# Kernel tuning notes

Hardware: AMD Instinct MI355X
Metric: run time of the kernel (lower is better)

## Reference

```python
import jax, jax.numpy as jnp
import numpy as np
from jax import lax

# MinkowskiEngine semantics reproduced on a dense grid:
# - a sparse tensor's active set = voxels where any feature channel is nonzero
# - stride-1 conv: output coords == input coords  -> mask output with input mask
# - stride-2 conv (k=5, pad=2): output coords = unique(floor(c/2))  -> 2x2x2 max-pool of mask
# - GlobalPooling: mean of features over active output coords, per batch
# MinkowskiConvolution has no bias by default; MinkowskiLinear has one.

DN = ('NCDHW', 'OIDHW', 'NCDHW')

def conv3d(x, w, stride, pad):
    return lax.conv_general_dilated(
        x, w, (stride, stride, stride), [(pad, pad)] * 3, dimension_numbers=DN)

def pool_mask(m):
    # occupancy of stride-2 output coords: any active voxel in each 2x2x2 block
    B, T, H, W = m.shape
    return m.reshape(B, T // 2, 2, H // 2, 2, W // 2, 2).max(axis=(2, 4, 6))

def setup_inputs() -> dict:
    key = jax.random.key(0)
    ks = jax.random.split(key, 7)
    B, T, C, H, W = 16, 128, 2, 34, 34
    vals = jax.random.normal(ks[0], (B, T, C, H, W), jnp.float32)
    keep = jax.random.bernoulli(ks[1], 0.05, (B, T, 1, H, W)).astype(jnp.float32)
    x = vals * keep
    w1 = jax.random.normal(ks[2], (32, 2, 5, 5, 5), jnp.float32) * 0.05
    w2 = jax.random.normal(ks[3], (64, 32, 5, 5, 5), jnp.float32) * 0.05
    w3 = jax.random.normal(ks[4], (128, 64, 3, 3, 3), jnp.float32) * 0.05
    wl = jax.random.normal(ks[5], (10, 128), jnp.float32) * 0.05
    bl = jnp.zeros((10,), jnp.float32)
    return {"x": x, "w1": w1, "w2": w2, "w3": w3, "wl": wl, "bl": bl}

def reference(x, w1, w2, w3, wl, bl):
    # x: [B, T, C, H, W] -> permute(0,2,1,3,4) -> [B, C, T, H, W]
    dense = jnp.transpose(x, (0, 2, 1, 3, 4))
    # active coordinate set of ME.to_sparse(dense)
    mask = (jnp.abs(dense).sum(axis=1) > 0).astype(dense.dtype)  # [B, T, H, W]
    mask = lax.stop_gradient(mask)
    m1 = mask[:, None]
    h = conv3d(dense, w1, 1, 2) * m1                         # k5 s1, out coords = in coords
    mask2 = pool_mask(mask)                                  # stride-2 output occupancy
    m2 = mask2[:, None]
    h = jax.nn.relu(conv3d(h, w2, 2, 2)) * m2                # k5 s2 + ReLU
    h = jax.nn.relu(conv3d(h, w3, 1, 1)) * m2                # k3 s1 + ReLU
    cnt = jnp.maximum(mask2.sum(axis=(1, 2, 3)), 1.0)[:, None]
    pooled = h.sum(axis=(2, 3, 4)) / cnt                     # global avg over active coords -> [B,128]
    logits = pooled @ wl.T + bl                              # MinkowskiLinear(128,10)
    return jax.nn.softmax(jax.nn.relu(logits), axis=-1)      # ReLU -> Softmax -> ToFeature [B,10]
```

## Files before the change

kernel.cpp:

```cpp
#include <hip/hip_runtime.h>

#define BB 16
#define TT 128
#define HH 34
#define WW 34
#define HWSZ (HH*WW)
#define NP1 (BB*TT*HH*WW)
#define TD 64
#define HD 17
#define WD 17
#define NP2 (BB*TD*HD*WD)
#define NW1 (NP1/64)
#define NW2 (NP2/64)
#define CAP1 262144
#define CAP2 131072

typedef __attribute__((ext_vector_type(8))) short bf16x8;
typedef __attribute__((ext_vector_type(4))) float f32x4;

__device__ inline unsigned short f2bf(float f) {
  unsigned u = __float_as_uint(f);
  unsigned r = (u + 0x7fff + ((u >> 16) & 1)) >> 16;
  return (unsigned short)r;
}
__device__ inline float bf2f(unsigned short s) {
  return __uint_as_float((unsigned)s << 16);
}

__global__ void k_ballot1(const float* __restrict__ x, unsigned long long* __restrict__ b1) {
  int i = blockIdx.x * 256 + threadIdx.x;
  int hw = i % HWSZ;
  int bt = i / HWSZ;
  const float* px = x + (size_t)bt * 2 * HWSZ + hw;
  bool act = (fabsf(px[0]) + fabsf(px[HWSZ])) > 0.0f;
  unsigned long long m = __ballot(act);
  if ((threadIdx.x & 63) == 0) b1[i >> 6] = m;
}

__global__ void k_ballot2(const unsigned long long* __restrict__ b1,
                          unsigned long long* __restrict__ b2) {
  int i = blockIdx.x * 256 + threadIdx.x;
  if (i >= NP2) return;
  int ow = i % WD; int r = i / WD;
  int oh = r % HD; r /= HD;
  int od = r % TD; int b = r / TD;
  bool act = false;
  for (int dt = 0; dt < 2; dt++)
    for (int dh = 0; dh < 2; dh++)
      for (int dw = 0; dw < 2; dw++) {
        int t = od * 2 + dt, h = oh * 2 + dh, w = ow * 2 + dw;
        int lin = ((b * TT + t) * HH + h) * WW + w;
        if ((b1[lin >> 6] >> (lin & 63)) & 1ull) act = true;
      }
  unsigned long long m = __ballot(act);
  if ((threadIdx.x & 63) == 0) b2[i >> 6] = m;
}

__global__ __launch_bounds__(1024) void k_scan(
    const unsigned long long* __restrict__ b1, const unsigned long long* __restrict__ b2,
    int* __restrict__ wb1, int* __restrict__ wb2,
    int* __restrict__ counter1, int* __restrict__ counter2, float* __restrict__ cnt) {
  __shared__ int wsum[16];
  __shared__ int wpre[16];
  __shared__ int tots[2];
  int tid = threadIdx.x, lane = tid & 63, wv = tid >> 6;

  const int CH1 = (NW1 + 1023) / 1024;
  int lo = tid * CH1, hi = min(lo + CH1, NW1);
  int s = 0;
  for (int i = lo; i < hi; i++) s += __popcll(b1[i]);
  int sc = s;
  #pragma unroll
  for (int d = 1; d < 64; d <<= 1) { int y = __shfl_up(sc, d); if (lane >= d) sc += y; }
  if (lane == 63) wsum[wv] = sc;
  __syncthreads();
  if (wv == 0 && lane < 16) {
    int v = wsum[lane];
    int p = v;
    #pragma unroll
    for (int d = 1; d < 16; d <<= 1) { int y = __shfl_up(p, d); if (lane >= d) p += y; }
    wpre[lane] = p - v;
    if (lane == 15) tots[0] = p;
  }
  __syncthreads();
  {
    int base = wpre[wv] + (sc - s);
    for (int i = lo; i < hi; i++) { wb1[i] = base; base += __popcll(b1[i]); }
  }
  if (tid == 0) *counter1 = tots[0];
  __syncthreads();

  const int CH2 = (NW2 + 1023) / 1024;
  lo = tid * CH2; hi = min(lo + CH2, NW2);
  s = 0;
  for (int i = lo; i < hi; i++) s += __popcll(b2[i]);
  sc = s;
  #pragma unroll
  for (int d = 1; d < 64; d <<= 1) { int y = __shfl_up(sc, d); if (lane >= d) sc += y; }
  if (lane == 63) wsum[wv] = sc;
  __syncthreads();
  if (wv == 0 && lane < 16) {
    int v = wsum[lane];
    int p = v;
    #pragma unroll
    for (int d = 1; d < 16; d <<= 1) { int y = __shfl_up(p, d); if (lane >= d) p += y; }
    wpre[lane] = p - v;
    if (lane == 15) tots[1] = p;
  }
  __syncthreads();
  {
    int base = wpre[wv] + (sc - s);
    for (int i = lo; i < hi; i++) { wb2[i] = base; base += __popcll(b2[i]); }
  }
  if (tid == 0) *counter2 = tots[1];
  __syncthreads();
  if (tid < 16) {
    int c0 = wb2[tid * 289];
    int c1 = (tid == 15) ? tots[1] : wb2[(tid + 1) * 289];
    cnt[tid] = (float)(c1 - c0);
  }
}

__global__ void k_fill1(const unsigned long long* __restrict__ b1,
                        const int* __restrict__ wb1, int* __restrict__ idx1) {
  int i = blockIdx.x * 256 + threadIdx.x;
  unsigned long long m = b1[i >> 6];
  int lane = i & 63;
  int p = -1;
  if ((m >> lane) & 1ull) {
    p = wb1[i >> 6] + __popcll(m & ((1ull << lane) - 1ull));
    if (p >= CAP1) p = -1;
  }
  idx1[i] = p;
}

__global__ void k_fill2(const unsigned long long* __restrict__ b2,
                        const int* __restrict__ wb2,
                        int* __restrict__ idx2, int* __restrict__ list2) {
  int i = blockIdx.x * 256 + threadIdx.x;
  if (i >= NP2) return;
  unsigned long long m = b2[i >> 6];
  int lane = i & 63;
  int p = -1;
  if ((m >> lane) & 1ull) {
    p = wb2[i >> 6] + __popcll(m & ((1ull << lane) - 1ull));
    if (p < CAP2) list2[p] = i; else p = -1;
  }
  idx2[i] = p;
}

__global__ __launch_bounds__(256) void k_conv1e(
    const float* __restrict__ x, const float* __restrict__ w1,
    const unsigned long long* __restrict__ b1, const int* __restrict__ wb1,
    unsigned short* __restrict__ h1c) {
  __shared__ unsigned short w1s[8000];
  __shared__ unsigned int plist[384];
  __shared__ unsigned long long q[4][128];
  __shared__ int pcnt;
  int tid = threadIdx.x;
  int b = blockIdx.x >> 7;
  int t0 = blockIdx.x & 127;
  if (tid == 0) pcnt = 0;
  for (int j = tid; j < 8000; j += 256) w1s[j] = f2bf(w1[j]);
  __syncthreads();
  int slabbase = (b * TT + t0) * HWSZ;
  for (int hw = tid; hw < HWSZ; hw += 256) {
    int lin = slabbase + hw;
    unsigned long long m = b1[lin >> 6];
    int ln = lin & 63;
    if ((m >> ln) & 1ull) {
      int p = wb1[lin >> 6] + __popcll(m & ((1ull << ln) - 1ull));
      if (p < CAP1) {
        int s = atomicAdd(&pcnt, 1);
        if (s < 384) plist[s] = ((unsigned)p << 11) | (unsigned)hw;
      }
    }
  }
  __syncthreads();
  int n = min(pcnt, 384);
  int lane = tid & 63, wid = tid >> 6;
  int oc = lane & 31, c = lane >> 5;
  int woff = (oc * 2 + c) * 125;
  int csh = c * 16;
  int kt = lane / 5, kh = lane - kt * 5;
  const float* xb = x + (size_t)b * TT * 2 * HWSZ;
  for (int li = wid; li < n; li += 4) {
    unsigned e = plist[li];
    int hw = e & 0x7ff;
    int p = e >> 11;
    int h_ = hw / 34, w_ = hw - h_ * 34;
    int cntA = 0;
    unsigned m5 = 0;
    int t2 = 0, h2 = 0;
    if (lane < 25) {
      t2 = t0 + kt - 2;
      h2 = h_ + kh - 2;
      if ((unsigned)t2 < TT && (unsigned)h2 < HH) {
        int kwmin = (w_ < 2) ? (2 - w_) : 0;
        int kwmax = (w_ > 31) ? (35 - w_) : 4;
        int lin = ((b * TT + t2) * HH + h2) * WW + (w_ + kwmin - 2);
        int wi = lin >> 6, sh = lin & 63;
        unsigned long long v = b1[wi] >> sh;
        if (sh > 59) v |= b1[wi + 1] << (64 - sh);
        m5 = ((unsigned)v & ((1u << (kwmax - kwmin + 1)) - 1u)) << kwmin;
        cntA = __popc(m5);
      }
    }
    int inc = cntA;
    #pragma unroll
    for (int d = 1; d < 64; d <<= 1) { int y = __shfl_up(inc, d); if (lane >= d) inc += y; }
    int off = inc - cntA;
    int ne = __shfl(inc, 63);
    unsigned mm = m5;
    while (mm) {
      int kw = __ffs(mm) - 1; mm &= mm - 1;
      int w2 = w_ + kw - 2;
      int xoff = (t2 * 2) * HWSZ + h2 * 34 + w2;
      unsigned short xv0 = f2bf(xb[xoff]);
      unsigned short xv1 = f2bf(xb[xoff + HWSZ]);
      int tap = (kt * 5 + kh) * 5 + kw;
      q[wid][off++] = (unsigned long long)((unsigned)xv0 | ((unsigned)xv1 << 16)) |
                      ((unsigned long long)tap << 32);
    }
    float acc = 0.f;
    for (int e2 = 0; e2 < ne; e2++) {
      unsigned long long ent = q[wid][e2];
      int tap = (int)(ent >> 32);
      float xv = bf2f((unsigned short)((ent >> csh) & 0xffffull));
      acc += xv * bf2f(w1s[woff + tap]);
    }
    float other = __shfl_down(acc, 32);
    if (lane < 32) h1c[(size_t)p * 32 + oc] = f2bf(acc + other);
  }
}

__global__ void k_tw2b(const float* __restrict__ w2, unsigned short* __restrict__ w2b) {
  int i = blockIdx.x * blockDim.x + threadIdx.x;
  if (i >= 125 * 64 * 32) return;
  int c = i & 31; int r = i >> 5;
  int oc = r & 63; int tap = r >> 6;
  w2b[i] = f2bf(w2[((size_t)oc * 32 + c) * 125 + tap]);
}
__global__ void k_tw3b(const float* __restrict__ w3, unsigned short* __restrict__ w3b) {
  int i = blockIdx.x * blockDim.x + threadIdx.x;
  if (i >= 27 * 128 * 64) return;
  int c = i & 63; int r = i >> 6;
  int oc = r & 127; int tap = r >> 7;
  w3b[i] = f2bf(w3[((size_t)oc * 64 + c) * 27 + tap]);
}

#define S2 40
__global__ __launch_bounds__(256) void k_conv2m(
    const unsigned short* __restrict__ h1c,
    const unsigned short* __restrict__ w2b,
    const int* __restrict__ idx1,
    const int* __restrict__ list2, const int* __restrict__ counter2,
    unsigned short* __restrict__ h2c) {
  __shared__ __align__(16) unsigned short As[2][64 * S2];
  __shared__ __align__(16) unsigned short Bs[2][64 * S2];
  __shared__ int rowsL[125 * 64];
  __shared__ int4 mc[64];
  int tid = threadIdx.x;
  int lane = tid & 63, wid = tid >> 6;
  int fr = lane & 15, fq = lane >> 4;
  int wr = (wid >> 1) * 32, wc = (wid & 1) * 32;
  int count2 = min(*counter2, CAP2);
  int nchunk = (count2 + 63) >> 6;
  int spos = tid >> 2, sq = tid & 3;
  for (int ch = blockIdx.x; ch < nchunk; ch += gridDim.x) {
    __syncthreads();
    if (tid < 64) {
      int p = ch * 64 + tid;
      int m = (p < count2) ? list2[p] : -1;
      int4 q; q.x = -1; q.y = 0; q.z = 0; q.w = 0;
      if (m >= 0) {
        int ow = m % WD; int r = m / WD;
        int oh = r % HD; r /= HD;
        q.x = r / TD; q.y = r % TD; q.z = oh; q.w = ow;
      }
      mc[tid] = q;
    }
    __syncthreads();
    for (int j = tid; j < 8000; j += 256) {
      int tap = j >> 6, pos = j & 63;
      int4 q = mc[pos];
      int row = -1;
      if (q.x >= 0) {
        int kt = tap / 25, r2 = tap - kt * 25;
        int kh = r2 / 5, kw = r2 - kh * 5;
        int t = q.y * 2 + kt - 2, h = q.z * 2 + kh - 2, w = q.w * 2 + kw - 2;
        if ((unsigned)t < TT && (unsigned)h < HH && (unsigned)w < WW)
          row = idx1[((q.x * TT + t) * HH + h) * WW + w];
      }
      rowsL[j] = row;
    }
    __syncthreads();
    f32x4 acc[2][2];
    #pragma unroll
    for (int i = 0; i < 2; i++)
      #pragma unroll
      for (int j = 0; j < 2; j++) acc[i][j] = (f32x4){0.f, 0.f, 0.f, 0.f};
    int4 rA = {0, 0, 0, 0};
    {
      int row = rowsL[spos];
      if (row >= 0) rA = *(const int4*)(h1c + (size_t)row * 32 + sq * 8);
    }
    int4 rB = *(const int4*)(w2b + (size_t)spos * 32 + sq * 8);
    for (int tap = 0; tap < 125; tap++) {
      int bsel = tap & 1;
      *(int4*)(&As[bsel][spos * S2 + sq * 8]) = rA;
      *(int4*)(&Bs[bsel][spos * S2 + sq * 8]) = rB;
      if (tap < 124) {
        int row = rowsL[(tap + 1) * 64 + spos];
        int4 v = {0, 0, 0, 0};
        if (row >= 0) v = *(const int4*)(h1c + (size_t)row * 32 + sq * 8);
        rA = v;
        rB = *(const int4*)(w2b + ((size_t)(tap + 1) * 64 + spos) * 32 + sq * 8);
      }
      __syncthreads();
      const unsigned short* ap = &As[bsel][(wr + fr) * S2 + fq * 8];
      const unsigned short* bp = &Bs[bsel][(wc + fr) * S2 + fq * 8];
      bf16x8 a0 = *(const bf16x8*)ap;
      bf16x8 a1 = *(const bf16x8*)(ap + 16 * S2);
      bf16x8 b0 = *(const bf16x8*)bp;
      bf16x8 b1 = *(const bf16x8*)(bp + 16 * S2);
      acc[0][0] = __builtin_amdgcn_mfma_f32_16x16x32_bf16(a0, b0, acc[0][0], 0, 0, 0);
      acc[0][1] = __builtin_amdgcn_mfma_f32_16x16x32_bf16(a0, b1, acc[0][1], 0, 0, 0);
      acc[1][0] = __builtin_amdgcn_mfma_f32_16x16x32_bf16(a1, b0, acc[1][0], 0, 0, 0);
      acc[1][1] = __builtin_amdgcn_mfma_f32_16x16x32_bf16(a1, b1, acc[1][1], 0, 0, 0);
    }
    int base = ch * 64;
    #pragma unroll
    for (int mi = 0; mi < 2; mi++)
      #pragma unroll
      for (int ni = 0; ni < 2; ni++)
        #pragma unroll
        for (int j = 0; j < 4; j++) {
          int r = wr + mi * 16 + fq * 4 + j;
          int p = base + r;
          if (p < count2) {
            int col = wc + ni * 16 + fr;
            h2c[(size_t)p * 64 + col] = f2bf(fmaxf(acc[mi][ni][j], 0.f));
          }
        }
  }
}

#define S3 72
#define SH3 132
__global__ __launch_bounds__(256) void k_conv3m(
    const unsigned short* __restrict__ h2c,
    const unsigned short* __restrict__ w3b,
    const int* __restrict__ idx2,
    const int* __restrict__ list2, const int* __restrict__ counter2,
    float* __restrict__ pooled) {
  __shared__ __align__(16) unsigned short As[2][64 * S3];
  __shared__ __align__(16) unsigned short Bs[2][128 * S3];
  __shared__ float pools[2048];
  __shared__ int rowsL[27 * 64];
  __shared__ int4 mc[64];
  __shared__ int posb[64];
  int tid = threadIdx.x;
  int lane = tid & 63, wid = tid >> 6;
  int fr = lane & 15, fq = lane >> 4;
  int wr = (wid >> 1) * 32, wc = (wid & 1) * 64;
  for (int j = tid; j < 2048; j += 256) pools[j] = 0.f;
  int count2 = min(*counter2, CAP2);
  int nchunk = (count2 + 63) >> 6;
  int spos = tid >> 2, sq = tid & 3;
  int boc = tid >> 1, bh = tid & 1;
  for (int ch = blockIdx.x; ch < nchunk; ch += gridDim.x) {
    __syncthreads();
    if (tid < 64) {
      int p = ch * 64 + tid;
      int m = (p < count2) ? list2[p] : -1;
      int4 q; q.x = -1; q.y = 0; q.z = 0; q.w = 0;
      if (m >= 0) {
        int ow = m % WD; int r = m / WD;
        int oh = r % HD; r /= HD;
        q.x = r / TD; q.y = r % TD; q.z = oh; q.w = ow;
      }
      mc[tid] = q;
      posb[tid] = (q.x >= 0) ? q.x : 0;
    }
    __syncthreads();
    for (int j = tid; j < 27 * 64; j += 256) {
      int tap = j >> 6, pos = j & 63;
      int4 q = mc[pos];
      int row = -1;
      if (q.x >= 0) {
        int dt = tap / 9 - 1, dh = (tap / 3) % 3 - 1, dw = tap % 3 - 1;
        int t = q.y + dt, h = q.z + dh, w = q.w + dw;
        if ((unsigned)t < TD && (unsigned)h < HD && (unsigned)w < WD)
          row = idx2[((q.x * TD + t) * HD + h) * WD + w];
      }
      rowsL[j] = row;
    }
    __syncthreads();
    f32x4 acc[2][4];
    #pragma unroll
    for (int i = 0; i < 2; i++)
      #pragma unroll
      for (int j = 0; j < 4; j++) acc[i][j] = (f32x4){0.f, 0.f, 0.f, 0.f};
    int4 rA0 = {0, 0, 0, 0}, rA1 = {0, 0, 0, 0};
    {
      int row = rowsL[spos];
      if (row >= 0) {
        const unsigned short* s = h2c + (size_t)row * 64 + sq * 16;
        rA0 = *(const int4*)s;
        rA1 = *(const int4*)(s + 8);
      }
    }
    int4 rB0, rB1, rB2, rB3;
    {
      const unsigned short* wsrc = w3b + (size_t)boc * 64 + bh * 32;
      rB0 = *(const int4*)(wsrc);
      rB1 = *(const int4*)(wsrc + 8);
      rB2 = *(const int4*)(wsrc + 16);
      rB3 = *(const int4*)(wsrc + 24);
    }
    for (int tap = 0; tap < 27; tap++) {
      int bsel = tap & 1;
      {
        unsigned short* ad = &As[bsel][spos * S3 + sq * 16];
        *(int4*)(ad) = rA0;
        *(int4*)(ad + 8) = rA1;
        unsigned short* bd = &Bs[bsel][boc * S3 + bh * 32];
        *(int4*)(bd) = rB0;
        *(int4*)(bd + 8) = rB1;
        *(int4*)(bd + 16) = rB2;
        *(int4*)(bd + 24) = rB3;
      }
      if (tap < 26) {
        int row = rowsL[(tap + 1) * 64 + spos];
        int4 v0 = {0, 0, 0, 0}, v1 = {0, 0, 0, 0};
        if (row >= 0) {
          const unsigned short* s = h2c + (size_t)row * 64 + sq * 16;
          v0 = *(const int4*)s;
          v1 = *(const int4*)(s + 8);
        }
        rA0 = v0; rA1 = v1;
        const unsigned short* wsrc = w3b + ((size_t)(tap + 1) * 128 + boc) * 64 + bh * 32;
        rB0 = *(const int4*)(wsrc);
        rB1 = *(const int4*)(wsrc + 8);
        rB2 = *(const int4*)(wsrc + 16);
        rB3 = *(const int4*)(wsrc + 24);
      }
      __syncthreads();
      const unsigned short* ap = &As[bsel][(wr + fr) * S3 + fq * 8];
      const unsigned short* bp = &Bs[bsel][(wc + fr) * S3 + fq * 8];
      #pragma unroll
      for (int kk = 0; kk < 2; kk++) {
        bf16x8 a0 = *(const bf16x8*)(ap + kk * 32);
        bf16x8 a1 = *(const bf16x8*)(ap + 16 * S3 + kk * 32);
        #pragma unroll
        for (int ni = 0; ni < 4; ni++) {
          bf16x8 bfrag = *(const bf16x8*)(bp + ni * 16 * S3 + kk * 32);
          acc[0][ni] = __builtin_amdgcn_mfma_f32_16x16x32_bf16(a0, bfrag, acc[0][ni], 0, 0, 0);
          acc[1][ni] = __builtin_amdgcn_mfma_f32_16x16x32_bf16(a1, bfrag, acc[1][ni], 0, 0, 0);
        }
      }
    }
    __syncthreads();
    unsigned short* h3 = &As[0][0];
    #pragma unroll
    for (int mi = 0; mi < 2; mi++)
      #pragma unroll
      for (int ni = 0; ni < 4; ni++)
        #pragma unroll
        for (int j = 0; j < 4; j++) {
          int r = wr + mi * 16 + fq * 4 + j;
          int col = wc + ni * 16 + fr;
          h3[r * SH3 + col] = f2bf(fmaxf(acc[mi][ni][j], 0.f));
        }
    __syncthreads();
    if (tid < 128) {
      for (int r = 0; r < 64; r++)
        pools[posb[r] * 128 + tid] += bf2f(h3[r * SH3 + tid]);
    }
  }
  __syncthreads();
  for (int j = tid; j < 2048; j += 256)
    atomicAdd(&pooled[j], pools[j]);
}

__global__ void k_final(const float* __restrict__ pooled, const float* __restrict__ cnt,
                        const float* __restrict__ wl, const float* __restrict__ bl,
                        float* __restrict__ out) {
  __shared__ float pr[128];
  __shared__ float lg[10];
  int b = blockIdx.x;
  int tid = threadIdx.x;
  float c = fmaxf(cnt[b], 1.0f);
  pr[tid] = pooled[b * 128 + tid] / c;
  __syncthreads();
  if (tid < 10) {
    float acc = bl[tid];
    for (int j = 0; j < 128; j++) acc += pr[j] * wl[tid * 128 + j];
    lg[tid] = fmaxf(acc, 0.f);
  }
  __syncthreads();
  if (tid == 0) {
    float mx = lg[0];
    for (int k = 1; k < 10; k++) mx = fmaxf(mx, lg[k]);
    float se = 0.f;
    for (int k = 0; k < 10; k++) se += expf(lg[k] - mx);
    for (int k = 0; k < 10; k++) out[b * 10 + k] = expf(lg[k] - mx) / se;
  }
}

extern "C" void kernel_launch(void* const* d_in, const int* in_sizes, int n_in,
                              void* d_out, int out_size, void* d_ws, size_t ws_size,
                              hipStream_t stream) {
  const float* x  = (const float*)d_in[0];
  const float* w1 = (const float*)d_in[1];
  const float* w2 = (const float*)d_in[2];
  const float* w3 = (const float*)d_in[3];
  const float* wl = (const float*)d_in[4];
  const float* bl = (const float*)d_in[5];
  float* out = (float*)d_out;

  float* ws = (float*)d_ws;
  int* counter1 = (int*)(ws + 0);
  int* counter2 = (int*)(ws + 1);
  float* cnt = ws + 16;
  float* pooled = ws + 32;
  size_t off = 2080;
  unsigned long long* b1 = (unsigned long long*)(ws + off); off += NW1 * 2 + 2;
  unsigned long long* b2 = (unsigned long long*)(ws + off); off += NW2 * 2;
  int* wb1 = (int*)(ws + off); off += NW1;
  int* wb2 = (int*)(ws + off); off += NW2;
  int* idx1 = (int*)(ws + off); off += NP1;
  unsigned short* h1c = (unsigned short*)(ws + off); off += (size_t)CAP1 * 16;
  int* idx2 = (int*)(ws + off); off += NP2;
  int* list2 = (int*)(ws + off); off += CAP2;
  unsigned short* h2c = (unsigned short*)(ws + off); off += (size_t)CAP2 * 32;
  unsigned short* w2b = (unsigned short*)(ws + off); off += 128000;
  unsigned short* w3b = (unsigned short*)(ws + off); off += 110592;

  hipMemsetAsync(d_ws, 0, 8448, stream);

  k_tw2b<<<(256000 + 255) / 256, 256, 0, stream>>>(w2, w2b);
  k_tw3b<<<(221184 + 255) / 256, 256, 0, stream>>>(w3, w3b);
  k_ballot1<<<NP1 / 256, 256, 0, stream>>>(x, b1);
  k_ballot2<<<(NP2 + 255) / 256, 256, 0, stream>>>(b1, b2);
  k_scan<<<1, 1024, 0, stream>>>(b1, b2, wb1, wb2, counter1, counter2, cnt);
  k_conv1e<<<2048, 256, 0, stream>>>(x, w1, b1, wb1, h1c);
  k_fill1<<<NP1 / 256, 256, 0, stream>>>(b1, wb1, idx1);
  k_fill2<<<(NP2 + 255) / 256, 256, 0, stream>>>(b2, wb2, idx2, list2);
  k_conv2m<<<1024, 256, 0, stream>>>(h1c, w2b, idx1, list2, counter2, h2c);
  k_conv3m<<<768, 256, 0, stream>>>(h2c, w3b, idx2, list2, counter2, pooled);
  k_final<<<16, 128, 0, stream>>>(pooled, cnt, wl, bl, out);
}
```

Baseline: 427.4 us.

## Process two taps per barrier in conv2, swizzle chunk mapping, drop pooling atomics

The conv2 inner loop now stages two kernel taps per synchronization using four LDS buffers. This halves the number of __syncthreads per chunk and gives more MFMA work between barriers. Both conv kernels remap block IDs to chunks with an XCD-style swizzle so that neighbouring chunks land on the same die. The conv3 pooled reduction now writes per-block partials instead of global atomics, and the final kernel reduces them with 1024 threads. The cost is more LDS in conv2 and an extra pass over 768x2048 partials in the final kernel.

```diff
diff --git a/kernel.cpp b/kernel.cpp
--- a/kernel.cpp
+++ b/kernel.cpp
@@ -14,6 +14,8 @@
 #define NW2 (NP2/64)
 #define CAP1 262144
 #define CAP2 131072
+#define G2 1024
+#define G3 768
 
 typedef __attribute__((ext_vector_type(8))) short bf16x8;
 typedef __attribute__((ext_vector_type(4))) float f32x4;
@@ -256,8 +258,8 @@
     const int* __restrict__ idx1,
     const int* __restrict__ list2, const int* __restrict__ counter2,
     unsigned short* __restrict__ h2c) {
-  __shared__ __align__(16) unsigned short As[2][64 * S2];
-  __shared__ __align__(16) unsigned short Bs[2][64 * S2];
+  __shared__ __align__(16) unsigned short As[4][64 * S2];
+  __shared__ __align__(16) unsigned short Bs[4][64 * S2];
   __shared__ int rowsL[125 * 64];
   __shared__ int4 mc[64];
   int tid = threadIdx.x;
@@ -267,7 +269,8 @@
   int count2 = min(*counter2, CAP2);
   int nchunk = (count2 + 63) >> 6;
   int spos = tid >> 2, sq = tid & 3;
-  for (int ch = blockIdx.x; ch < nchunk; ch += gridDim.x) {
+  int chid = (blockIdx.x & 7) * (G2 >> 3) + (blockIdx.x >> 3);
+  for (int ch = chid; ch < nchunk; ch += gridDim.x) {
     __syncthreads();
     if (tid < 64) {
       int p = ch * 64 + tid;
@@ -300,34 +303,45 @@
     for (int i = 0; i < 2; i++)
       #pragma unroll
       for (int j = 0; j < 2; j++) acc[i][j] = (f32x4){0.f, 0.f, 0.f, 0.f};
-    int4 rA = {0, 0, 0, 0};
+    int4 rA0 = {0,0,0,0}, rA1 = {0,0,0,0};
     {
-      int row = rowsL[spos];
-      if (row >= 0) rA = *(const int4*)(h1c + (size_t)row * 32 + sq * 8);
-    }
-    int4 rB = *(const int4*)(w2b + (size_t)spos * 32 + sq * 8);
-    for (int tap = 0; tap < 125; tap++) {
-      int bsel = tap & 1;
-      *(int4*)(&As[bsel][spos * S2 + sq * 8]) = rA;
-      *(int4*)(&Bs[bsel][spos * S2 + sq * 8]) = rB;
-      if (tap < 124) {
-        int row = rowsL[(tap + 1) * 64 + spos];
-        int4 v = {0, 0, 0, 0};
-        if (row >= 0) v = *(const int4*)(h1c + (size_t)row * 32 + sq * 8);
-        rA = v;
-        rB = *(const int4*)(w2b + ((size_t)(tap + 1) * 64 + spos) * 32 + sq * 8);
-      }
+      int r0 = rowsL[spos];
+      int r1 = rowsL[64 + spos];
+      if (r0 >= 0) rA0 = *(const int4*)(h1c + (size_t)r0 * 32 + sq * 8);
+      if (r1 >= 0) rA1 = *(const int4*)(h1c + (size_t)r1 * 32 + sq * 8);
+    }
+    int4 rB0 = *(const int4*)(w2b + (size_t)spos * 32 + sq * 8);
+    int4 rB1 = *(const int4*)(w2b + (size_t)(64 + spos) * 32 + sq * 8);
+    for (int pg = 0; pg < 63; ++pg) {
+      int sl = (pg & 1) * 2;
+      *(int4*)(&As[sl + 0][spos * S2 + sq * 8]) = rA0;
+      *(int4*)(&As[sl + 1][spos * S2 + sq * 8]) = rA1;
+      *(int4*)(&Bs[sl + 0][spos * S2 + sq * 8]) = rB0;
+      *(int4*)(&Bs[sl + 1][spos * S2 + sq * 8]) = rB1;
       __syncthreads();
-      const unsigned short* ap = &As[bsel][(wr + fr) * S2 + fq * 8];
-      const unsigned short* bp = &Bs[bsel][(wc + fr) * S2 + fq * 8];
-      bf16x8 a0 = *(const bf16x8*)ap;
-      bf16x8 a1 = *(const bf16x8*)(ap + 16 * S2);
-      bf16x8 b0 = *(const bf16x8*)bp;
-      bf16x8 b1 = *(const bf16x8*)(bp + 16 * S2);
-      acc[0][0] = __builtin_amdgcn_mfma_f32_16x16x32_bf16(a0, b0, acc[0][0], 0, 0, 0);
-      acc[0][1] = __builtin_amdgcn_mfma_f32_16x16x32_bf16(a0, b1, acc[0][1], 0, 0, 0);
-      acc[1][0] = __builtin_amdgcn_mfma_f32_16x16x32_bf16(a1, b0, acc[1][0], 0, 0, 0);
-      acc[1][1] = __builtin_amdgcn_mfma_f32_16x16x32_bf16(a1, b1, acc[1][1], 0, 0, 0);
+      if (pg < 62) {
+        int t0 = 2 * pg + 2, t1 = 2 * pg + 3;
+        int r0 = rowsL[t0 * 64 + spos];
+        int r1 = (t1 <= 124) ? rowsL[t1 * 64 + spos] : -1;
+        rA0 = make_int4(0,0,0,0); rA1 = make_int4(0,0,0,0);
+        if (r0 >= 0) rA0 = *(const int4*)(h1c + (size_t)r0 * 32 + sq * 8);
+        if (r1 >= 0) rA1 = *(const int4*)(h1c + (size_t)r1 * 32 + sq * 8);
+        rB0 = *(const int4*)(w2b + (size_t)t0 * 2048 + spos * 32 + sq * 8);
+        rB1 = *(const int4*)(w2b + (size_t)min(t1, 124) * 2048 + spos * 32 + sq * 8);
+      }
+      #pragma unroll
+      for (int t = 0; t < 2; t++) {
+        const unsigned short* ap = &As[sl + t][(wr + fr) * S2 + fq * 8];
+        const unsigned short* bp = &Bs[sl + t][(wc + fr) * S2 + fq * 8];
+        bf16x8 a0 = *(const bf16x8*)ap;
+        bf16x8 a1 = *(const bf16x8*)(ap + 16 * S2);
+        bf16x8 b0 = *(const bf16x8*)bp;
+        bf16x8 b1 = *(const bf16x8*)(bp + 16 * S2);
+        acc[0][0] = __builtin_amdgcn_mfma_f32_16x16x32_bf16(a0, b0, acc[0][0], 0, 0, 0);
+        acc[0][1] = __builtin_amdgcn_mfma_f32_16x16x32_bf16(a0, b1, acc[0][1], 0, 0, 0);
+        acc[1][0] = __builtin_amdgcn_mfma_f32_16x16x32_bf16(a1, b0, acc[1][0], 0, 0, 0);
+        acc[1][1] = __builtin_amdgcn_mfma_f32_16x16x32_bf16(a1, b1, acc[1][1], 0, 0, 0);
+      }
     }
     int base = ch * 64;
     #pragma unroll
@@ -353,7 +367,7 @@
     const unsigned short* __restrict__ w3b,
     const int* __restrict__ idx2,
     const int* __restrict__ list2, const int* __restrict__ counter2,
-    float* __restrict__ pooled) {
+    float* __restrict__ partial) {
   __shared__ __align__(16) unsigned short As[2][64 * S3];
   __shared__ __align__(16) unsigned short Bs[2][128 * S3];
   __shared__ float pools[2048];
@@ -369,7 +383,8 @@
   int nchunk = (count2 + 63) >> 6;
   int spos = tid >> 2, sq = tid & 3;
   int boc = tid >> 1, bh = tid & 1;
-  for (int ch = blockIdx.x; ch < nchunk; ch += gridDim.x) {
+  int chid = (blockIdx.x & 7) * (G3 >> 3) + (blockIdx.x >> 3);
+  for (int ch = chid; ch < nchunk; ch += gridDim.x) {
     __syncthreads();
     if (tid < 64) {
       int p = ch * 64 + tid;
@@ -481,18 +496,29 @@
   }
   __syncthreads();
   for (int j = tid; j < 2048; j += 256)
-    atomicAdd(&pooled[j], pools[j]);
-}
-
-__global__ void k_final(const float* __restrict__ pooled, const float* __restrict__ cnt,
-                        const float* __restrict__ wl, const float* __restrict__ bl,
-                        float* __restrict__ out) {
+    partial[(size_t)blockIdx.x * 2048 + j] = pools[j];
+}
+
+__global__ __launch_bounds__(1024) void k_final(
+    const float* __restrict__ partial, const float* __restrict__ cnt,
+    const float* __restrict__ wl, const float* __restrict__ bl,
+    float* __restrict__ out) {
+  __shared__ float red[1024];
   __shared__ float pr[128];
   __shared__ float lg[10];
   int b = blockIdx.x;
   int tid = threadIdx.x;
-  float c = fmaxf(cnt[b], 1.0f);
-  pr[tid] = pooled[b * 128 + tid] / c;
+  int c = tid & 127, sl = tid >> 7;
+  float s = 0.f;
+  for (int g = sl; g < G3; g += 8) s += partial[(size_t)g * 2048 + b * 128 + c];
+  red[tid] = s;
+  __syncthreads();
+  if (tid < 128) {
+    float t = 0.f;
+    #pragma unroll
+    for (int k = 0; k < 8; k++) t += red[k * 128 + tid];
+    pr[tid] = t / fmaxf(cnt[b], 1.0f);
+  }
   __syncthreads();
   if (tid < 10) {
     float acc = bl[tid];
@@ -524,7 +550,6 @@
   int* counter1 = (int*)(ws + 0);
   int* counter2 = (int*)(ws + 1);
   float* cnt = ws + 16;
-  float* pooled = ws + 32;
   size_t off = 2080;
   unsigned long long* b1 = (unsigned long long*)(ws + off); off += NW1 * 2 + 2;
   unsigned long long* b2 = (unsigned long long*)(ws + off); off += NW2 * 2;
@@ -537,8 +562,9 @@
   unsigned short* h2c = (unsigned short*)(ws + off); off += (size_t)CAP2 * 32;
   unsigned short* w2b = (unsigned short*)(ws + off); off += 128000;
   unsigned short* w3b = (unsigned short*)(ws + off); off += 110592;
-
-  hipMemsetAsync(d_ws, 0, 8448, stream);
+  float* partial = ws + off; off += (size_t)G3 * 2048;
+
+  hipMemsetAsync(d_ws, 0, 256, stream);
 
   k_tw2b<<<(256000 + 255) / 256, 256, 0, stream>>>(w2, w2b);
   k_tw3b<<<(221184 + 255) / 256, 256, 0, stream>>>(w3, w3b);
@@ -548,7 +574,7 @@
   k_conv1e<<<2048, 256, 0, stream>>>(x, w1, b1, wb1, h1c);
   k_fill1<<<NP1 / 256, 256, 0, stream>>>(b1, wb1, idx1);
   k_fill2<<<(NP2 + 255) / 256, 256, 0, stream>>>(b2, wb2, idx2, list2);
-  k_conv2m<<<1024, 256, 0, stream>>>(h1c, w2b, idx1, list2, counter2, h2c);
-  k_conv3m<<<768, 256, 0, stream>>>(h2c, w3b, idx2, list2, counter2, pooled);
-  k_final<<<16, 128, 0, stream>>>(pooled, cnt, wl, bl, out);
-}
+  k_conv2m<<<G2, 256, 0, stream>>>(h1c, w2b, idx1, list2, counter2, h2c);
+  k_conv3m<<<G3, 256, 0, stream>>>(h2c, w3b, idx2, list2, counter2, partial);
+  k_final<<<16, 1024, 0, stream>>>(partial, cnt, wl, bl, out);
+}
```

After: 505.8 us. 1.18x slower.
